# Performance work log

Hardware: AMD Instinct MI355X
Metric: run time of the kernel (lower is better)

Reference implementation:

```python
import jax, jax.numpy as jnp
import numpy as np

N_HEADS = 32
N_KV = 16
HEAD_DIM = 128
REPEATS = N_HEADS // N_KV
ROPE_THETA = 10000.0
SOFTCAP = 50.0
SCALE = 1.0 / np.sqrt(144.0)


def _rope_cos_sin(L, dtype):
    half = HEAD_DIM // 2
    inv_freq = 1.0 / (ROPE_THETA ** (jnp.arange(0, HEAD_DIM, 2, dtype=jnp.float32) / HEAD_DIM))
    ang = jnp.arange(L, dtype=jnp.float32)[:, None] * inv_freq[None, :]  # [L, half]
    return jnp.cos(ang).astype(dtype), jnp.sin(ang).astype(dtype)


def _apply_rope(t, cos, sin):
    # t: [B, H, L, D]; non-traditional (rotate-half) RoPE
    half = HEAD_DIM // 2
    t1, t2 = t[..., :half], t[..., half:]
    c = cos[None, None, :, :]
    s = sin[None, None, :, :]
    return jnp.concatenate([t1 * c - t2 * s, t2 * c + t1 * s], axis=-1)


def setup_inputs() -> dict:
    key = jax.random.key(0)
    k1, k2, k3, k4, k5 = jax.random.split(key, 5)
    B, L, D = 1, 2048, 4608
    x = jax.random.normal(k1, (B, L, D), dtype=jnp.float32)
    wq = jax.random.normal(k2, (N_HEADS * HEAD_DIM, D), dtype=jnp.float32) * 0.02
    wk = jax.random.normal(k3, (N_KV * HEAD_DIM, D), dtype=jnp.float32) * 0.02
    wv = jax.random.normal(k4, (N_KV * HEAD_DIM, D), dtype=jnp.float32) * 0.02
    wo = jax.random.normal(k5, (D, N_HEADS * HEAD_DIM), dtype=jnp.float32) * 0.02
    mask = jnp.tril(jnp.ones((L, L), dtype=bool))  # causal
    return {"x": x, "mask": mask, "wq": wq, "wk": wk, "wv": wv, "wo": wo}


def reference(x, mask, wq, wk, wv, wo):
    B, L, D = x.shape
    q = (x @ wq.T).reshape(B, L, N_HEADS, HEAD_DIM).transpose(0, 2, 1, 3)
    k = (x @ wk.T).reshape(B, L, N_KV, HEAD_DIM).transpose(0, 2, 1, 3)
    v = (x @ wv.T).reshape(B, L, N_KV, HEAD_DIM).transpose(0, 2, 1, 3)

    cos, sin = _rope_cos_sin(L, x.dtype)
    q = _apply_rope(q, cos, sin) * jnp.asarray(SCALE, x.dtype)
    k = _apply_rope(k, cos, sin)

    # GQA: group queries per kv head -> [B, n_kv, repeats, L, D]
    qg = q.reshape(B, N_KV, REPEATS, L, HEAD_DIM)
    scores = jnp.einsum("bgrqd,bgkd->bgrqk", qg, k)
    scores = jnp.tanh(scores / SOFTCAP) * SOFTCAP
    neg = jnp.asarray(jnp.finfo(scores.dtype).min, scores.dtype)
    scores = jnp.where(mask[None, None, None, :, :], scores, neg)
    probs = jax.nn.softmax(scores, axis=-1)
    out = jnp.einsum("bgrqk,bgkd->bgrqd", probs, v)  # [B, n_kv, rep, L, D]
    out = out.reshape(B, N_HEADS, L, HEAD_DIM).transpose(0, 2, 1, 3).reshape(B, L, -1)
    return out @ wo.T
```

## Files before the change

### kernel.cpp

```cpp
#include <hip/hip_runtime.h>
#include <hip/hip_bf16.h>
#include <math.h>

typedef unsigned short u16;
typedef __attribute__((ext_vector_type(8))) short s16x8;
typedef __attribute__((ext_vector_type(4))) float f32x4;

#define SCALE 0.083333333333333329f
#define SOFTCAP_INV 0.02f

__device__ __forceinline__ u16 f2bf(float f) {
    unsigned u = __float_as_uint(f);
    unsigned r = 0x7fffu + ((u >> 16) & 1u);
    return (u16)((u + r) >> 16);
}
__device__ __forceinline__ float bf2f(u16 v) {
    return __uint_as_float(((unsigned)v) << 16);
}

__device__ __forceinline__ float fast_tanh(float x) {
    float e = __expf(2.0f * x);
    return 1.0f - 2.0f / (e + 1.0f);
}

__global__ __launch_bounds__(256) void cast_kernel(const float* __restrict__ in,
                                                   u16* __restrict__ out) {
    size_t i = ((size_t)blockIdx.x * 256 + threadIdx.x) * 4;
    float4 v = *(const float4*)(in + i);
    ushort4 o;
    o.x = f2bf(v.x); o.y = f2bf(v.y); o.z = f2bf(v.z); o.w = f2bf(v.w);
    *(ushort4*)(out + i) = o;
}

__global__ __launch_bounds__(256) void rope_table_kernel(float* __restrict__ cosT,
                                                         float* __restrict__ sinT) {
    int idx = blockIdx.x * 256 + threadIdx.x;
    int i = idx & 63, pos = idx >> 6;
    float inv = __expf(-((float)i / 64.0f) * 9.210340371976184f);
    float ang = (float)pos * inv;
    cosT[idx] = cosf(ang);
    sinT[idx] = sinf(ang);
}

__global__ __launch_bounds__(256) void rope_q_kernel(const u16* __restrict__ T16,
                                                     u16* __restrict__ Qb,
                                                     const float* __restrict__ cosT,
                                                     const float* __restrict__ sinT) {
    int idx = blockIdx.x * 256 + threadIdx.x;
    int i = idx & 63;
    int head = (idx >> 6) & 31;
    int pos = idx >> 11;
    size_t rbase = (size_t)pos * 8192 + head * 128 + i;
    float t1 = bf2f(T16[rbase]), t2 = bf2f(T16[rbase + 64]);
    float c = cosT[(pos << 6) + i], s = sinT[(pos << 6) + i];
    size_t wbase = (size_t)pos * 4096 + head * 128 + i;
    Qb[wbase]      = f2bf((t1 * c - t2 * s) * SCALE);
    Qb[wbase + 64] = f2bf((t2 * c + t1 * s) * SCALE);
}

__global__ __launch_bounds__(256) void rope_k_kernel(const u16* __restrict__ T16,
                                                     u16* __restrict__ Kb,
                                                     const float* __restrict__ cosT,
                                                     const float* __restrict__ sinT) {
    int idx = blockIdx.x * 256 + threadIdx.x;
    int i = idx & 63;
    int head = (idx >> 6) & 15;
    int pos = idx >> 10;
    size_t rbase = (size_t)pos * 8192 + 4096 + head * 128 + i;
    float t1 = bf2f(T16[rbase]), t2 = bf2f(T16[rbase + 64]);
    float c = cosT[(pos << 6) + i], s = sinT[(pos << 6) + i];
    size_t wbase = (size_t)pos * 2048 + head * 128 + i;
    Kb[wbase]      = f2bf(t1 * c - t2 * s);
    Kb[wbase + 64] = f2bf(t2 * c + t1 * s);
}

__global__ __launch_bounds__(256) void vtrans_kernel(const u16* __restrict__ T16,
                                                     u16* __restrict__ Vt) {
    __shared__ u16 tile[32][33];
    int bc = (blockIdx.x & 63) << 5;
    int bl = (blockIdx.x >> 6) << 5;
    int x = threadIdx.x & 31, y = threadIdx.x >> 5;
    #pragma unroll
    for (int yy = y; yy < 32; yy += 8)
        tile[yy][x] = T16[(size_t)(bl + yy) * 8192 + 6144 + bc + x];
    __syncthreads();
    #pragma unroll
    for (int yy = y; yy < 32; yy += 8)
        Vt[(size_t)(bc + yy) * 2048 + bl + x] = tile[x][yy];
}

#define STAGE_A(buf, ktt, l)                                                            \
    __builtin_amdgcn_global_load_lds(                                                   \
        (const __attribute__((address_space(1))) unsigned int*)(aSrc + (size_t)(ktt) * 64 + (size_t)(l) * 64 * K), \
        (__attribute__((address_space(3))) unsigned int*)(&lds[buf][0][(l) * 4096 + ldsoff]), 16, 0, 0)
#define STAGE_B(buf, ktt, l)                                                            \
    __builtin_amdgcn_global_load_lds(                                                   \
        (const __attribute__((address_space(1))) unsigned int*)(bSrc + (size_t)(ktt) * 64 + (size_t)(l) * 64 * K), \
        (__attribute__((address_space(3))) unsigned int*)(&lds[buf][1][(l) * 4096 + ldsoff]), 16, 0, 0)

template<bool OUT_BF16>
__device__ __forceinline__ void gemm256_core(const u16* __restrict__ A,
                                             const u16* __restrict__ B,
                                             void* __restrict__ C,
                                             int N, int K, int kbeg, int nt,
                                             int bm, int bn,
                                             u16 (&lds)[2][2][16384]) {
    int t = threadIdx.x;
    int lane = t & 63, wave = t >> 6;
    int wm = wave >> 2, wn = wave & 3;
    int fr = lane & 15, fq = lane >> 4;
    int sw = (fr & 7) << 4;

    int srow = wave * 8 + (lane >> 3);
    int scb = ((lane & 7) * 16) ^ (((lane >> 3) & 7) << 4);
    const u16* aSrc = A + (size_t)(bm * 256 + srow) * K + kbeg + (scb >> 1);
    const u16* bSrc = B + (size_t)(bn * 256 + srow) * K + kbeg + (scb >> 1);
    int ldsoff = wave * 512;

    f32x4 acc[8][4];
    #pragma unroll
    for (int m = 0; m < 8; m++)
        #pragma unroll
        for (int n = 0; n < 4; n++)
            acc[m][n] = (f32x4){0.f, 0.f, 0.f, 0.f};

    STAGE_B(0, 0, 0); STAGE_B(0, 0, 1); STAGE_B(0, 0, 2); STAGE_B(0, 0, 3);
    STAGE_A(0, 0, 0); STAGE_A(0, 0, 2); STAGE_A(0, 0, 1); STAGE_A(0, 0, 3);

    for (int it = 0; it < nt; ++it) {
        int cur = it & 1, nxt = cur ^ 1;
        bool more = (it + 1 < nt);
        const char* Ab = (const char*)&lds[cur][0][0];
        const char* Bb = (const char*)&lds[cur][1][0];
        int cb0 = (fq * 16) ^ sw;
        int cb1 = (64 + fq * 16) ^ sw;

        if (more) {
            STAGE_B(nxt, it + 1, 0); STAGE_B(nxt, it + 1, 1);
            __builtin_amdgcn_sched_barrier(0);
            asm volatile("s_waitcnt vmcnt(4)" ::: "memory");
        } else {
            asm volatile("s_waitcnt vmcnt(2)" ::: "memory");
        }
        __builtin_amdgcn_s_barrier();
        s16x8 b0[4], a0[4];
        #pragma unroll
        for (int n = 0; n < 4; ++n)
            b0[n] = *(const s16x8*)(Bb + (wn * 64 + n * 16 + fr) * 128 + cb0);
        #pragma unroll
        for (int m = 0; m < 4; ++m)
            a0[m] = *(const s16x8*)(Ab + (wm * 128 + m * 16 + fr) * 128 + cb0);
        __builtin_amdgcn_s_setprio(1);
        #pragma unroll
        for (int m = 0; m < 4; ++m)
            #pragma unroll
            for (int n = 0; n < 4; ++n)
                acc[m][n] = __builtin_amdgcn_mfma_f32_16x16x32_bf16(a0[m], b0[n], acc[m][n], 0, 0, 0);
        __builtin_amdgcn_s_setprio(0);
        __builtin_amdgcn_s_barrier();

        if (more) {
            STAGE_B(nxt, it + 1, 2); STAGE_B(nxt, it + 1, 3);
            __builtin_amdgcn_sched_barrier(0);
            asm volatile("s_waitcnt vmcnt(4)" ::: "memory");
        } else {
            asm volatile("s_waitcnt vmcnt(0)" ::: "memory");
        }
        __builtin_amdgcn_s_barrier();
        s16x8 a1[4];
        #pragma unroll
        for (int m = 0; m < 4; ++m)
            a1[m] = *(const s16x8*)(Ab + (wm * 128 + (4 + m) * 16 + fr) * 128 + cb0);
        __builtin_amdgcn_s_setprio(1);
        #pragma unroll
        for (int m = 0; m < 4; ++m)
            #pragma unroll
            for (int n = 0; n < 4; ++n)
                acc[4 + m][n] = __builtin_amdgcn_mfma_f32_16x16x32_bf16(a1[m], b0[n], acc[4 + m][n], 0, 0, 0);
        __builtin_amdgcn_s_setprio(0);
        __builtin_amdgcn_s_barrier();

        if (more) { STAGE_A(nxt, it + 1, 0); STAGE_A(nxt, it + 1, 2); }
        s16x8 b1[4], a2[4];
        #pragma unroll
        for (int n = 0; n < 4; ++n)
            b1[n] = *(const s16x8*)(Bb + (wn * 64 + n * 16 + fr) * 128 + cb1);
        #pragma unroll
        for (int m = 0; m < 4; ++m)
            a2[m] = *(const s16x8*)(Ab + (wm * 128 + m * 16 + fr) * 128 + cb1);
        __builtin_amdgcn_s_setprio(1);
        #pragma unroll
        for (int m = 0; m < 4; ++m)
            #pragma unroll
            for (int n = 0; n < 4; ++n)
                acc[m][n] = __builtin_amdgcn_mfma_f32_16x16x32_bf16(a2[m], b1[n], acc[m][n], 0, 0, 0);
        __builtin_amdgcn_s_setprio(0);
        __builtin_amdgcn_s_barrier();

        if (more) { STAGE_A(nxt, it + 1, 1); STAGE_A(nxt, it + 1, 3); }
        s16x8 a3[4];
        #pragma unroll
        for (int m = 0; m < 4; ++m)
            a3[m] = *(const s16x8*)(Ab + (wm * 128 + (4 + m) * 16 + fr) * 128 + cb1);
        __builtin_amdgcn_s_setprio(1);
        #pragma unroll
        for (int m = 0; m < 4; ++m)
            #pragma unroll
            for (int n = 0; n < 4; ++n)
                acc[4 + m][n] = __builtin_amdgcn_mfma_f32_16x16x32_bf16(a3[m], b1[n], acc[4 + m][n], 0, 0, 0);
        __builtin_amdgcn_s_setprio(0);
        __builtin_amdgcn_s_barrier();
    }

    #pragma unroll
    for (int m = 0; m < 8; ++m) {
        int row = bm * 256 + wm * 128 + m * 16 + fq * 4;
        #pragma unroll
        for (int n = 0; n < 4; ++n) {
            int col = bn * 256 + wn * 64 + n * 16 + fr;
            #pragma unroll
            for (int r = 0; r < 4; ++r) {
                if (OUT_BF16) ((u16*)C)[(size_t)(row + r) * N + col] = f2bf(acc[m][n][r]);
                else          ((float*)C)[(size_t)(row + r) * N + col] = acc[m][n][r];
            }
        }
    }
}

__global__ __launch_bounds__(512) void gemm256_qkv(const u16* __restrict__ A,
                                                   const u16* __restrict__ B,
                                                   u16* __restrict__ C, int K) {
    __shared__ u16 lds[2][2][16384];
    int bid = blockIdx.x;
    int x = bid & 7, j = bid >> 3;
    int bn = x * 4 + (j & 3);
    int bm = j >> 2;
    gemm256_core<true>(A, B, C, 8192, K, 0, K >> 6, bm, bn, lds);
}

__global__ __launch_bounds__(512) void gemm256_out(const u16* __restrict__ A,
                                                   const u16* __restrict__ B,
                                                   float* __restrict__ C, int K) {
    __shared__ u16 lds[2][2][16384];
    int bid = blockIdx.x;
    int j = (bid & 7) * 18 + (bid >> 3);
    int bm = j & 7;
    int bn = j >> 3;
    gemm256_core<false>(A, B, C, 4608, K, 0, K >> 6, bm, bn, lds);
}

__global__ __launch_bounds__(256) void attn_kernel(const u16* __restrict__ Qb,
                                                   const u16* __restrict__ Kb,
                                                   const u16* __restrict__ Vt,
                                                   u16* __restrict__ Ob) {
    __shared__ u16 Ks[64 * 128];
    __shared__ u16 Vs[128 * 64];
    __shared__ u16 Pst[4 * 1024];

    int bid = blockIdx.x;
    int hq = bid & 31;
    int qb = 31 - (bid >> 5);
    int g = hq >> 1;
    int t = threadIdx.x;
    int lane = t & 63, wave = t >> 6;
    int fr = lane & 15, fq = lane >> 4;
    int sw = (fr & 7) << 4;
    int qrow0 = qb * 64 + wave * 16;
    u16* Pw = &Pst[wave * 1024];

    s16x8 qf[4];
    #pragma unroll
    for (int s = 0; s < 4; s++)
        qf[s] = *(const s16x8*)&Qb[(size_t)(qrow0 + fr) * 4096 + hq * 128 + s * 32 + fq * 8];

    f32x4 o[8];
    #pragma unroll
    for (int c = 0; c < 8; c++) o[c] = (f32x4){0.f, 0.f, 0.f, 0.f};
    float mi[4] = {-INFINITY, -INFINITY, -INFINITY, -INFINITY};
    float li[4] = {0.f, 0.f, 0.f, 0.f};

    int w4 = wave * 4;
    int nT = qb + 1;
    for (int kt = 0; kt < nT; kt++) {
        int kv0 = kt << 6;
        __syncthreads();
        #pragma unroll
        for (int i = 0; i < 4; i++) {
            int li_ = w4 + i;
            int rk = li_ * 4 + (lane >> 4);
            int cbk = ((lane & 15) * 16) ^ ((rk & 7) << 4);
            const u16* srcK = Kb + (size_t)(kv0 + rk) * 2048 + g * 128 + (cbk >> 1);
            __builtin_amdgcn_global_load_lds(
                (const __attribute__((address_space(1))) unsigned int*)srcK,
                (__attribute__((address_space(3))) unsigned int*)(Ks + li_ * 512), 16, 0, 0);
            int rv = li_ * 8 + (lane >> 3);
            int cbv = ((lane & 7) * 16) ^ ((rv & 7) << 4);
            const u16* srcV = Vt + (size_t)(g * 128 + rv) * 2048 + kv0 + (cbv >> 1);
            __builtin_amdgcn_global_load_lds(
                (const __attribute__((address_space(1))) unsigned int*)srcV,
                (__attribute__((address_space(3))) unsigned int*)(Vs + li_ * 512), 16, 0, 0);
        }
        __syncthreads();

        if (kv0 <= qrow0 + 15) {
            f32x4 sf[4];
            #pragma unroll
            for (int j = 0; j < 4; j++) sf[j] = (f32x4){0.f, 0.f, 0.f, 0.f};
            #pragma unroll
            for (int j = 0; j < 4; j++)
                #pragma unroll
                for (int s = 0; s < 4; s++) {
                    s16x8 kf = *(const s16x8*)&Ks[(j * 16 + fr) * 128 + (((s * 64 + fq * 16) ^ sw) >> 1)];
                    sf[j] = __builtin_amdgcn_mfma_f32_16x16x32_bf16(qf[s], kf, sf[j], 0, 0, 0);
                }
            float pmax[4] = {-INFINITY, -INFINITY, -INFINITY, -INFINITY};
            #pragma unroll
            for (int j = 0; j < 4; j++)
                #pragma unroll
                for (int r = 0; r < 4; r++) {
                    float sc = 50.f * fast_tanh(sf[j][r] * SOFTCAP_INV);
                    int colk = kv0 + j * 16 + fr;
                    int rowq = qrow0 + fq * 4 + r;
                    sc = (colk > rowq) ? -INFINITY : sc;
                    sf[j][r] = sc;
                    pmax[r] = fmaxf(pmax[r], sc);
                }
            #pragma unroll
            for (int d = 1; d < 16; d <<= 1)
                #pragma unroll
                for (int r = 0; r < 4; r++)
                    pmax[r] = fmaxf(pmax[r], __shfl_xor(pmax[r], d));
            float al[4], psum[4] = {0.f, 0.f, 0.f, 0.f};
            #pragma unroll
            for (int r = 0; r < 4; r++) {
                float mn = fmaxf(mi[r], pmax[r]);
                al[r] = __expf(mi[r] - mn);
                mi[r] = mn;
            }
            #pragma unroll
            for (int j = 0; j < 4; j++)
                #pragma unroll
                for (int r = 0; r < 4; r++) {
                    float p = __expf(sf[j][r] - mi[r]);
                    sf[j][r] = p;
                    psum[r] += p;
                }
            #pragma unroll
            for (int d = 1; d < 16; d <<= 1)
                #pragma unroll
                for (int r = 0; r < 4; r++)
                    psum[r] += __shfl_xor(psum[r], d);
            #pragma unroll
            for (int r = 0; r < 4; r++)
                li[r] = li[r] * al[r] + psum[r];
            #pragma unroll
            for (int c = 0; c < 8; c++)
                #pragma unroll
                for (int r = 0; r < 4; r++)
                    o[c][r] *= al[r];
            #pragma unroll
            for (int j = 0; j < 4; j++)
                #pragma unroll
                for (int r = 0; r < 4; r++) {
                    int row = fq * 4 + r, col = j * 16 + fr;
                    int byteoff = (row * 128 + col * 2) ^ ((row & 7) << 4);
                    *(u16*)((char*)Pw + byteoff) = f2bf(sf[j][r]);
                }
            #pragma unroll
            for (int s = 0; s < 2; s++) {
                int rbyte = (fr * 128 + s * 64 + fq * 16) ^ sw;
                s16x8 pf = *(const s16x8*)((const char*)Pw + rbyte);
                #pragma unroll
                for (int c = 0; c < 8; c++) {
                    s16x8 vf = *(const s16x8*)&Vs[(c * 16 + fr) * 64 + (((s * 64 + fq * 16) ^ sw) >> 1)];
                    o[c] = __builtin_amdgcn_mfma_f32_16x16x32_bf16(pf, vf, o[c], 0, 0, 0);
                }
            }
        }
    }
    #pragma unroll
    for (int c = 0; c < 8; c++)
        #pragma unroll
        for (int r = 0; r < 4; r++) {
            int rowq = qrow0 + fq * 4 + r;
            Ob[(size_t)rowq * 4096 + hq * 128 + c * 16 + fr] = f2bf(o[c][r] / li[r]);
        }
}

extern "C" void kernel_launch(void* const* d_in, const int* in_sizes, int n_in,
                              void* d_out, int out_size, void* d_ws, size_t ws_size,
                              hipStream_t stream) {
    const float* x  = (const float*)d_in[0];
    const float* wq = (const float*)d_in[2];
    const float* wk = (const float*)d_in[3];
    const float* wv = (const float*)d_in[4];
    const float* wo = (const float*)d_in[5];
    float* out = (float*)d_out;

    char* w = (char*)d_ws;
    u16*   xb   = (u16*)(w);
    u16*   wb   = (u16*)(w + 18874368);
    u16*   T16  = (u16*)(w + 94371840);
    u16*   Ob   = (u16*)(w + 127926272);
    u16*   Qbuf = (u16*)(w + 144703488);
    u16*   Kbuf = (u16*)(w + 161480704);
    u16*   Vt   = (u16*)(w + 169869312);
    float* cosT = (float*)(w + 178257920);
    float* sinT = (float*)(w + 178782208);

    rope_table_kernel<<<512, 256, 0, stream>>>(cosT, sinT);
    cast_kernel<<<9216, 256, 0, stream>>>(x, xb);

    cast_kernel<<<18432, 256, 0, stream>>>(wq, wb);
    cast_kernel<<<9216, 256, 0, stream>>>(wk, wb + (size_t)4096 * 4608);
    cast_kernel<<<9216, 256, 0, stream>>>(wv, wb + (size_t)6144 * 4608);

    gemm256_qkv<<<256, 512, 0, stream>>>(xb, wb, T16, 4608);

    rope_q_kernel<<<16384, 256, 0, stream>>>(T16, Qbuf, cosT, sinT);
    rope_k_kernel<<<8192, 256, 0, stream>>>(T16, Kbuf, cosT, sinT);
    vtrans_kernel<<<4096, 256, 0, stream>>>(T16, Vt);

    attn_kernel<<<1024, 256, 0, stream>>>(Qbuf, Kbuf, Vt, Ob);

    cast_kernel<<<18432, 256, 0, stream>>>(wo, wb);
    gemm256_out<<<144, 512, 0, stream>>>(Ob, wb, out, 4096);
}
```

Measured before the change: 464.7 us.

## Fuse RoPE into QKV GEMM epilogue and double-buffer attention K/V tiles

New measurement: 479.5 us. 1.03x slower.

```diff
diff --git a/kernel.cpp b/kernel.cpp
--- a/kernel.cpp
+++ b/kernel.cpp
@@ -13,9 +13,6 @@
     unsigned u = __float_as_uint(f);
     unsigned r = 0x7fffu + ((u >> 16) & 1u);
     return (u16)((u + r) >> 16);
-}
-__device__ __forceinline__ float bf2f(u16 v) {
-    return __uint_as_float(((unsigned)v) << 16);
 }
 
 __device__ __forceinline__ float fast_tanh(float x) {
@@ -32,49 +29,15 @@
     *(ushort4*)(out + i) = o;
 }
 
-__global__ __launch_bounds__(256) void rope_table_kernel(float* __restrict__ cosT,
-                                                         float* __restrict__ sinT) {
+__global__ __launch_bounds__(256) void rope_table_kernel(float2* __restrict__ csT) {
     int idx = blockIdx.x * 256 + threadIdx.x;
     int i = idx & 63, pos = idx >> 6;
     float inv = __expf(-((float)i / 64.0f) * 9.210340371976184f);
     float ang = (float)pos * inv;
-    cosT[idx] = cosf(ang);
-    sinT[idx] = sinf(ang);
-}
-
-__global__ __launch_bounds__(256) void rope_q_kernel(const u16* __restrict__ T16,
-                                                     u16* __restrict__ Qb,
-                                                     const float* __restrict__ cosT,
-                                                     const float* __restrict__ sinT) {
-    int idx = blockIdx.x * 256 + threadIdx.x;
-    int i = idx & 63;
-    int head = (idx >> 6) & 31;
-    int pos = idx >> 11;
-    size_t rbase = (size_t)pos * 8192 + head * 128 + i;
-    float t1 = bf2f(T16[rbase]), t2 = bf2f(T16[rbase + 64]);
-    float c = cosT[(pos << 6) + i], s = sinT[(pos << 6) + i];
-    size_t wbase = (size_t)pos * 4096 + head * 128 + i;
-    Qb[wbase]      = f2bf((t1 * c - t2 * s) * SCALE);
-    Qb[wbase + 64] = f2bf((t2 * c + t1 * s) * SCALE);
-}
-
-__global__ __launch_bounds__(256) void rope_k_kernel(const u16* __restrict__ T16,
-                                                     u16* __restrict__ Kb,
-                                                     const float* __restrict__ cosT,
-                                                     const float* __restrict__ sinT) {
-    int idx = blockIdx.x * 256 + threadIdx.x;
-    int i = idx & 63;
-    int head = (idx >> 6) & 15;
-    int pos = idx >> 10;
-    size_t rbase = (size_t)pos * 8192 + 4096 + head * 128 + i;
-    float t1 = bf2f(T16[rbase]), t2 = bf2f(T16[rbase + 64]);
-    float c = cosT[(pos << 6) + i], s = sinT[(pos << 6) + i];
-    size_t wbase = (size_t)pos * 2048 + head * 128 + i;
-    Kb[wbase]      = f2bf(t1 * c - t2 * s);
-    Kb[wbase + 64] = f2bf(t2 * c + t1 * s);
-}
-
-__global__ __launch_bounds__(256) void vtrans_kernel(const u16* __restrict__ T16,
+    csT[idx] = make_float2(cosf(ang), sinf(ang));
+}
+
+__global__ __launch_bounds__(256) void vtrans_kernel(const u16* __restrict__ Vraw,
                                                      u16* __restrict__ Vt) {
     __shared__ u16 tile[32][33];
     int bc = (blockIdx.x & 63) << 5;
@@ -82,7 +45,7 @@
     int x = threadIdx.x & 31, y = threadIdx.x >> 5;
     #pragma unroll
     for (int yy = y; yy < 32; yy += 8)
-        tile[yy][x] = T16[(size_t)(bl + yy) * 8192 + 6144 + bc + x];
+        tile[yy][x] = Vraw[(size_t)(bl + yy) * 2048 + bc + x];
     __syncthreads();
     #pragma unroll
     for (int yy = y; yy < 32; yy += 8)
@@ -98,16 +61,15 @@
         (const __attribute__((address_space(1))) unsigned int*)(bSrc + (size_t)(ktt) * 64 + (size_t)(l) * 64 * K), \
         (__attribute__((address_space(3))) unsigned int*)(&lds[buf][1][(l) * 4096 + ldsoff]), 16, 0, 0)
 
-template<bool OUT_BF16>
-__device__ __forceinline__ void gemm256_core(const u16* __restrict__ A,
+__device__ __forceinline__ void gemm256_loop(const u16* __restrict__ A,
                                              const u16* __restrict__ B,
-                                             void* __restrict__ C,
-                                             int N, int K, int kbeg, int nt,
+                                             int K, int kbeg, int nt,
                                              int bm, int bn,
-                                             u16 (&lds)[2][2][16384]) {
+                                             u16 (&lds)[2][2][16384],
+                                             f32x4 (&acc)[4][8]) {
     int t = threadIdx.x;
     int lane = t & 63, wave = t >> 6;
-    int wm = wave >> 2, wn = wave & 3;
+    int wm = wave >> 1, wn = wave & 1;
     int fr = lane & 15, fq = lane >> 4;
     int sw = (fr & 7) << 4;
 
@@ -117,15 +79,14 @@
     const u16* bSrc = B + (size_t)(bn * 256 + srow) * K + kbeg + (scb >> 1);
     int ldsoff = wave * 512;
 
-    f32x4 acc[8][4];
-    #pragma unroll
-    for (int m = 0; m < 8; m++)
-        #pragma unroll
-        for (int n = 0; n < 4; n++)
+    #pragma unroll
+    for (int m = 0; m < 4; m++)
+        #pragma unroll
+        for (int n = 0; n < 8; n++)
             acc[m][n] = (f32x4){0.f, 0.f, 0.f, 0.f};
 
-    STAGE_B(0, 0, 0); STAGE_B(0, 0, 1); STAGE_B(0, 0, 2); STAGE_B(0, 0, 3);
-    STAGE_A(0, 0, 0); STAGE_A(0, 0, 2); STAGE_A(0, 0, 1); STAGE_A(0, 0, 3);
+    STAGE_A(0, 0, 0); STAGE_A(0, 0, 1); STAGE_A(0, 0, 2); STAGE_A(0, 0, 3);
+    STAGE_B(0, 0, 0); STAGE_B(0, 0, 2); STAGE_B(0, 0, 1); STAGE_B(0, 0, 3);
 
     for (int it = 0; it < nt; ++it) {
         int cur = it & 1, nxt = cur ^ 1;
@@ -136,20 +97,20 @@
         int cb1 = (64 + fq * 16) ^ sw;
 
         if (more) {
-            STAGE_B(nxt, it + 1, 0); STAGE_B(nxt, it + 1, 1);
+            STAGE_A(nxt, it + 1, 0); STAGE_A(nxt, it + 1, 1);
             __builtin_amdgcn_sched_barrier(0);
             asm volatile("s_waitcnt vmcnt(4)" ::: "memory");
         } else {
             asm volatile("s_waitcnt vmcnt(2)" ::: "memory");
         }
         __builtin_amdgcn_s_barrier();
-        s16x8 b0[4], a0[4];
+        s16x8 a0[4], b0[4];
+        #pragma unroll
+        for (int m = 0; m < 4; ++m)
+            a0[m] = *(const s16x8*)(Ab + (wm * 64 + m * 16 + fr) * 128 + cb0);
         #pragma unroll
         for (int n = 0; n < 4; ++n)
-            b0[n] = *(const s16x8*)(Bb + (wn * 64 + n * 16 + fr) * 128 + cb0);
-        #pragma unroll
-        for (int m = 0; m < 4; ++m)
-            a0[m] = *(const s16x8*)(Ab + (wm * 128 + m * 16 + fr) * 128 + cb0);
+            b0[n] = *(const s16x8*)(Bb + (wn * 128 + n * 16 + fr) * 128 + cb0);
         __builtin_amdgcn_s_setprio(1);
         #pragma unroll
         for (int m = 0; m < 4; ++m)
@@ -160,82 +121,116 @@
         __builtin_amdgcn_s_barrier();
 
         if (more) {
-            STAGE_B(nxt, it + 1, 2); STAGE_B(nxt, it + 1, 3);
+            STAGE_A(nxt, it + 1, 2); STAGE_A(nxt, it + 1, 3);
             __builtin_amdgcn_sched_barrier(0);
             asm volatile("s_waitcnt vmcnt(4)" ::: "memory");
         } else {
             asm volatile("s_waitcnt vmcnt(0)" ::: "memory");
         }
         __builtin_amdgcn_s_barrier();
-        s16x8 a1[4];
-        #pragma unroll
-        for (int m = 0; m < 4; ++m)
-            a1[m] = *(const s16x8*)(Ab + (wm * 128 + (4 + m) * 16 + fr) * 128 + cb0);
+        s16x8 b1[4];
+        #pragma unroll
+        for (int n = 0; n < 4; ++n)
+            b1[n] = *(const s16x8*)(Bb + (wn * 128 + (4 + n) * 16 + fr) * 128 + cb0);
         __builtin_amdgcn_s_setprio(1);
         #pragma unroll
         for (int m = 0; m < 4; ++m)
             #pragma unroll
             for (int n = 0; n < 4; ++n)
-                acc[4 + m][n] = __builtin_amdgcn_mfma_f32_16x16x32_bf16(a1[m], b0[n], acc[4 + m][n], 0, 0, 0);
+                acc[m][4 + n] = __builtin_amdgcn_mfma_f32_16x16x32_bf16(a0[m], b1[n], acc[m][4 + n], 0, 0, 0);
         __builtin_amdgcn_s_setprio(0);
         __builtin_amdgcn_s_barrier();
 
-        if (more) { STAGE_A(nxt, it + 1, 0); STAGE_A(nxt, it + 1, 2); }
-        s16x8 b1[4], a2[4];
+        if (more) { STAGE_B(nxt, it + 1, 0); STAGE_B(nxt, it + 1, 2); }
+        s16x8 a2[4], b2[4];
+        #pragma unroll
+        for (int m = 0; m < 4; ++m)
+            a2[m] = *(const s16x8*)(Ab + (wm * 64 + m * 16 + fr) * 128 + cb1);
         #pragma unroll
         for (int n = 0; n < 4; ++n)
-            b1[n] = *(const s16x8*)(Bb + (wn * 64 + n * 16 + fr) * 128 + cb1);
-        #pragma unroll
-        for (int m = 0; m < 4; ++m)
-            a2[m] = *(const s16x8*)(Ab + (wm * 128 + m * 16 + fr) * 128 + cb1);
+            b2[n] = *(const s16x8*)(Bb + (wn * 128 + n * 16 + fr) * 128 + cb1);
         __builtin_amdgcn_s_setprio(1);
         #pragma unroll
         for (int m = 0; m < 4; ++m)
             #pragma unroll
             for (int n = 0; n < 4; ++n)
-                acc[m][n] = __builtin_amdgcn_mfma_f32_16x16x32_bf16(a2[m], b1[n], acc[m][n], 0, 0, 0);
+                acc[m][n] = __builtin_amdgcn_mfma_f32_16x16x32_bf16(a2[m], b2[n], acc[m][n], 0, 0, 0);
         __builtin_amdgcn_s_setprio(0);
         __builtin_amdgcn_s_barrier();
 
-        if (more) { STAGE_A(nxt, it + 1, 1); STAGE_A(nxt, it + 1, 3); }
-        s16x8 a3[4];
-        #pragma unroll
-        for (int m = 0; m < 4; ++m)
-            a3[m] = *(const s16x8*)(Ab + (wm * 128 + (4 + m) * 16 + fr) * 128 + cb1);
+        if (more) { STAGE_B(nxt, it + 1, 1); STAGE_B(nxt, it + 1, 3); }
+        s16x8 b3[4];
+        #pragma unroll
+        for (int n = 0; n < 4; ++n)
+            b3[n] = *(const s16x8*)(Bb + (wn * 128 + (4 + n) * 16 + fr) * 128 + cb1);
         __builtin_amdgcn_s_setprio(1);
         #pragma unroll
         for (int m = 0; m < 4; ++m)
             #pragma unroll
             for (int n = 0; n < 4; ++n)
-                acc[4 + m][n] = __builtin_amdgcn_mfma_f32_16x16x32_bf16(a3[m], b1[n], acc[4 + m][n], 0, 0, 0);
+                acc[m][4 + n] = __builtin_amdgcn_mfma_f32_16x16x32_bf16(a2[m], b3[n], acc[m][4 + n], 0, 0, 0);
         __builtin_amdgcn_s_setprio(0);
         __builtin_amdgcn_s_barrier();
-    }
-
-    #pragma unroll
-    for (int m = 0; m < 8; ++m) {
-        int row = bm * 256 + wm * 128 + m * 16 + fq * 4;
-        #pragma unroll
-        for (int n = 0; n < 4; ++n) {
-            int col = bn * 256 + wn * 64 + n * 16 + fr;
-            #pragma unroll
-            for (int r = 0; r < 4; ++r) {
-                if (OUT_BF16) ((u16*)C)[(size_t)(row + r) * N + col] = f2bf(acc[m][n][r]);
-                else          ((float*)C)[(size_t)(row + r) * N + col] = acc[m][n][r];
-            }
-        }
     }
 }
 
 __global__ __launch_bounds__(512) void gemm256_qkv(const u16* __restrict__ A,
                                                    const u16* __restrict__ B,
-                                                   u16* __restrict__ C, int K) {
+                                                   u16* __restrict__ Qb,
+                                                   u16* __restrict__ Kb,
+                                                   u16* __restrict__ Vraw,
+                                                   const float2* __restrict__ csT,
+                                                   int K) {
     __shared__ u16 lds[2][2][16384];
     int bid = blockIdx.x;
     int x = bid & 7, j = bid >> 3;
     int bn = x * 4 + (j & 3);
     int bm = j >> 2;
-    gemm256_core<true>(A, B, C, 8192, K, 0, K >> 6, bm, bn, lds);
+    f32x4 acc[4][8];
+    gemm256_loop(A, B, K, 0, K >> 6, bm, bn, lds, acc);
+
+    int lane = threadIdx.x & 63, wave = threadIdx.x >> 6;
+    int wm = wave >> 1, wn = wave & 1;
+    int fr = lane & 15, fq = lane >> 4;
+    int rowbase = bm * 256 + wm * 64 + fq * 4;
+
+    if (bn < 24) {
+        #pragma unroll
+        for (int m = 0; m < 4; ++m)
+            #pragma unroll
+            for (int n = 0; n < 4; ++n) {
+                int i = n * 16 + fr;
+                #pragma unroll
+                for (int r = 0; r < 4; ++r) {
+                    int pos = rowbase + m * 16 + r;
+                    float2 cs = csT[(pos << 6) + i];
+                    float t1 = acc[m][n][r], t2 = acc[m][n + 4][r];
+                    float o1 = t1 * cs.x - t2 * cs.y;
+                    float o2 = t2 * cs.x + t1 * cs.y;
+                    if (bn < 16) {
+                        int head = bn * 2 + wn;
+                        size_t base = (size_t)pos * 4096 + head * 128 + i;
+                        Qb[base]      = f2bf(o1 * SCALE);
+                        Qb[base + 64] = f2bf(o2 * SCALE);
+                    } else {
+                        int hk = (bn - 16) * 2 + wn;
+                        size_t base = (size_t)pos * 2048 + hk * 128 + i;
+                        Kb[base]      = f2bf(o1);
+                        Kb[base + 64] = f2bf(o2);
+                    }
+                }
+            }
+    } else {
+        #pragma unroll
+        for (int m = 0; m < 4; ++m)
+            #pragma unroll
+            for (int n = 0; n < 8; ++n) {
+                int colv = (bn - 24) * 256 + wn * 128 + n * 16 + fr;
+                #pragma unroll
+                for (int r = 0; r < 4; ++r)
+                    Vraw[(size_t)(rowbase + m * 16 + r) * 2048 + colv] = f2bf(acc[m][n][r]);
+            }
+    }
 }
 
 __global__ __launch_bounds__(512) void gemm256_out(const u16* __restrict__ A,
@@ -246,15 +241,31 @@
     int j = (bid & 7) * 18 + (bid >> 3);
     int bm = j & 7;
     int bn = j >> 3;
-    gemm256_core<false>(A, B, C, 4608, K, 0, K >> 6, bm, bn, lds);
+    f32x4 acc[4][8];
+    gemm256_loop(A, B, K, 0, K >> 6, bm, bn, lds, acc);
+
+    int lane = threadIdx.x & 63, wave = threadIdx.x >> 6;
+    int wm = wave >> 1, wn = wave & 1;
+    int fr = lane & 15, fq = lane >> 4;
+    #pragma unroll
+    for (int m = 0; m < 4; ++m) {
+        int row = bm * 256 + wm * 64 + m * 16 + fq * 4;
+        #pragma unroll
+        for (int n = 0; n < 8; ++n) {
+            int col = bn * 256 + wn * 128 + n * 16 + fr;
+            #pragma unroll
+            for (int r = 0; r < 4; ++r)
+                C[(size_t)(row + r) * 4608 + col] = acc[m][n][r];
+        }
+    }
 }
 
 __global__ __launch_bounds__(256) void attn_kernel(const u16* __restrict__ Qb,
                                                    const u16* __restrict__ Kb,
                                                    const u16* __restrict__ Vt,
                                                    u16* __restrict__ Ob) {
-    __shared__ u16 Ks[64 * 128];
-    __shared__ u16 Vs[128 * 64];
+    __shared__ u16 Ks[2][64 * 128];
+    __shared__ u16 Vs[2][128 * 64];
     __shared__ u16 Pst[4 * 1024];
 
     int bid = blockIdx.x;
@@ -267,6 +278,7 @@
     int sw = (fr & 7) << 4;
     int qrow0 = qb * 64 + wave * 16;
     u16* Pw = &Pst[wave * 1024];
+    int w4 = wave * 4;
 
     s16x8 qf[4];
     #pragma unroll
@@ -279,30 +291,56 @@
     float mi[4] = {-INFINITY, -INFINITY, -INFINITY, -INFINITY};
     float li[4] = {0.f, 0.f, 0.f, 0.f};
 
-    int w4 = wave * 4;
     int nT = qb + 1;
+
+    #pragma unroll
+    for (int i = 0; i < 4; i++) {
+        int li_ = w4 + i;
+        int rk = li_ * 4 + (lane >> 4);
+        int cbk = ((lane & 15) * 16) ^ ((rk & 7) << 4);
+        const u16* srcK = Kb + (size_t)rk * 2048 + g * 128 + (cbk >> 1);
+        __builtin_amdgcn_global_load_lds(
+            (const __attribute__((address_space(1))) unsigned int*)srcK,
+            (__attribute__((address_space(3))) unsigned int*)(&Ks[0][li_ * 512]), 16, 0, 0);
+        int rv = li_ * 8 + (lane >> 3);
+        int cbv = ((lane & 7) * 16) ^ ((rv & 7) << 4);
+        const u16* srcV = Vt + (size_t)(g * 128 + rv) * 2048 + (cbv >> 1);
+        __builtin_amdgcn_global_load_lds(
+            (const __attribute__((address_space(1))) unsigned int*)srcV,
+            (__attribute__((address_space(3))) unsigned int*)(&Vs[0][li_ * 512]), 16, 0, 0);
+    }
+
     for (int kt = 0; kt < nT; kt++) {
         int kv0 = kt << 6;
-        __syncthreads();
-        #pragma unroll
-        for (int i = 0; i < 4; i++) {
-            int li_ = w4 + i;
-            int rk = li_ * 4 + (lane >> 4);
-            int cbk = ((lane & 15) * 16) ^ ((rk & 7) << 4);
-            const u16* srcK = Kb + (size_t)(kv0 + rk) * 2048 + g * 128 + (cbk >> 1);
-            __builtin_amdgcn_global_load_lds(
-                (const __attribute__((address_space(1))) unsigned int*)srcK,
-                (__attribute__((address_space(3))) unsigned int*)(Ks + li_ * 512), 16, 0, 0);
-            int rv = li_ * 8 + (lane >> 3);
-            int cbv = ((lane & 7) * 16) ^ ((rv & 7) << 4);
-            const u16* srcV = Vt + (size_t)(g * 128 + rv) * 2048 + kv0 + (cbv >> 1);
-            __builtin_amdgcn_global_load_lds(
-                (const __attribute__((address_space(1))) unsigned int*)srcV,
-                (__attribute__((address_space(3))) unsigned int*)(Vs + li_ * 512), 16, 0, 0);
-        }
-        __syncthreads();
+        int cur = kt & 1, nxt = cur ^ 1;
+        if (kt + 1 < nT) {
+            int kvn = (kt + 1) << 6;
+            #pragma unroll
+            for (int i = 0; i < 4; i++) {
+                int li_ = w4 + i;
+                int rk = li_ * 4 + (lane >> 4);
+                int cbk = ((lane & 15) * 16) ^ ((rk & 7) << 4);
+                const u16* srcK = Kb + (size_t)(kvn + rk) * 2048 + g * 128 + (cbk >> 1);
+                __builtin_amdgcn_global_load_lds(
+                    (const __attribute__((address_space(1))) unsigned int*)srcK,
+                    (__attribute__((address_space(3))) unsigned int*)(&Ks[nxt][li_ * 512]), 16, 0, 0);
+                int rv = li_ * 8 + (lane >> 3);
+                int cbv = ((lane & 7) * 16) ^ ((rv & 7) << 4);
+                const u16* srcV = Vt + (size_t)(g * 128 + rv) * 2048 + kvn + (cbv >> 1);
+                __builtin_amdgcn_global_load_lds(
+                    (const __attribute__((address_space(1))) unsigned int*)srcV,
+                    (__attribute__((address_space(3))) unsigned int*)(&Vs[nxt][li_ * 512]), 16, 0, 0);
+            }
+            __builtin_amdgcn_sched_barrier(0);
+            asm volatile("s_waitcnt vmcnt(8)" ::: "memory");
+        } else {
+            asm volatile("s_waitcnt vmcnt(0)" ::: "memory");
+        }
+        __builtin_amdgcn_s_barrier();
 
         if (kv0 <= qrow0 + 15) {
+            const u16* Kc = &Ks[cur][0];
+            const u16* Vc = &Vs[cur][0];
             f32x4 sf[4];
             #pragma unroll
             for (int j = 0; j < 4; j++) sf[j] = (f32x4){0.f, 0.f, 0.f, 0.f};
@@ -310,7 +348,7 @@
             for (int j = 0; j < 4; j++)
                 #pragma unroll
                 for (int s = 0; s < 4; s++) {
-                    s16x8 kf = *(const s16x8*)&Ks[(j * 16 + fr) * 128 + (((s * 64 + fq * 16) ^ sw) >> 1)];
+                    s16x8 kf = *(const s16x8*)&Kc[(j * 16 + fr) * 128 + (((s * 64 + fq * 16) ^ sw) >> 1)];
                     sf[j] = __builtin_amdgcn_mfma_f32_16x16x32_bf16(qf[s], kf, sf[j], 0, 0, 0);
                 }
             float pmax[4] = {-INFINITY, -INFINITY, -INFINITY, -INFINITY};
@@ -372,11 +410,12 @@
                 s16x8 pf = *(const s16x8*)((const char*)Pw + rbyte);
                 #pragma unroll
                 for (int c = 0; c < 8; c++) {
-                    s16x8 vf = *(const s16x8*)&Vs[(c * 16 + fr) * 64 + (((s * 64 + fq * 16) ^ sw) >> 1)];
+                    s16x8 vf = *(const s16x8*)&Vc[(c * 16 + fr) * 64 + (((s * 64 + fq * 16) ^ sw) >> 1)];
                     o[c] = __builtin_amdgcn_mfma_f32_16x16x32_bf16(pf, vf, o[c], 0, 0, 0);
                 }
             }
         }
+        __builtin_amdgcn_s_barrier();
     }
     #pragma unroll
     for (int c = 0; c < 8; c++)
@@ -398,28 +437,25 @@
     float* out = (float*)d_out;
 
     char* w = (char*)d_ws;
-    u16*   xb   = (u16*)(w);
-    u16*   wb   = (u16*)(w + 18874368);
-    u16*   T16  = (u16*)(w + 94371840);
-    u16*   Ob   = (u16*)(w + 127926272);
-    u16*   Qbuf = (u16*)(w + 144703488);
-    u16*   Kbuf = (u16*)(w + 161480704);
-    u16*   Vt   = (u16*)(w + 169869312);
-    float* cosT = (float*)(w + 178257920);
-    float* sinT = (float*)(w + 178782208);
-
-    rope_table_kernel<<<512, 256, 0, stream>>>(cosT, sinT);
+    u16*    xb   = (u16*)(w);
+    u16*    wb   = (u16*)(w + 18874368);
+    u16*    Vraw = (u16*)(w + 94371840);
+    u16*    Ob   = (u16*)(w + 102760448);
+    u16*    Qbuf = (u16*)(w + 119537664);
+    u16*    Kbuf = (u16*)(w + 136314880);
+    u16*    Vt   = (u16*)(w + 144703488);
+    float2* csT  = (float2*)(w + 153092096);
+
+    rope_table_kernel<<<512, 256, 0, stream>>>(csT);
     cast_kernel<<<9216, 256, 0, stream>>>(x, xb);
 
     cast_kernel<<<18432, 256, 0, stream>>>(wq, wb);
     cast_kernel<<<9216, 256, 0, stream>>>(wk, wb + (size_t)4096 * 4608);
     cast_kernel<<<9216, 256, 0, stream>>>(wv, wb + (size_t)6144 * 4608);
 
-    gemm256_qkv<<<256, 512, 0, stream>>>(xb, wb, T16, 4608);
-
-    rope_q_kernel<<<16384, 256, 0, stream>>>(T16, Qbuf, cosT, sinT);
-    rope_k_kernel<<<8192, 256, 0, stream>>>(T16, Kbuf, cosT, sinT);
-    vtrans_kernel<<<4096, 256, 0, stream>>>(T16, Vt);
+    gemm256_qkv<<<256, 512, 0, stream>>>(xb, wb, Qbuf, Kbuf, Vraw, csT, 4608);
+
+    vtrans_kernel<<<4096, 256, 0, stream>>>(Vraw, Vt);
 
     attn_kernel<<<1024, 256, 0, stream>>>(Qbuf, Kbuf, Vt, Ob);
 
```
